# Kernel tuning notes

Measured on AMD Instinct MI355X. Metric: run time of the kernel, lower is better.

The kernel has to match this reference:

```python
import jax, jax.numpy as jnp
import numpy as np

TEMPERATURE = 0.5  # init temperature; attn_drop=0.0 so dropout is identity


def setup_inputs() -> dict:
    key = jax.random.key(0)
    k1, k2, k3 = jax.random.split(key, 3)
    B, H, N, D = 4, 8, 2048, 64
    q = jax.random.normal(k1, (B, H, N, D), dtype=jnp.float32)
    k = jax.random.normal(k2, (B, H, N, D), dtype=jnp.float32)
    v = jax.random.normal(k3, (B, H, N, D), dtype=jnp.float32)
    scale = jnp.asarray(D ** -0.5, dtype=jnp.float32)
    return {"q": q, "k": k, "v": v, "scale": scale}


def reference(q, k, v, scale):
    # logits: [B,H,N,N]
    logits = jnp.einsum("bhqd,bhkd->bhqk", q, k) * scale
    # first softmax acts as a soft mask over keys
    soft_mask = jax.nn.softmax(logits / TEMPERATURE, axis=-1)
    # second softmax over masked logits (elementwise product, NOT matmul)
    attn = jax.nn.softmax(logits * soft_mask, axis=-1)
    # dropout with p=0.0 is identity
    out = jnp.einsum("bhqk,bhkd->bhqd", attn, v)
    return out
```

## Files before the change

kernel.cpp:

```cpp
#include <hip/hip_runtime.h>


typedef _Float16 f16;
typedef f16 f16x8 __attribute__((ext_vector_type(8)));
typedef float f32x4 __attribute__((ext_vector_type(4)));

#define MFMA(a, b, c) __builtin_amdgcn_mfma_f32_16x16x32_f16((a), (b), (c), 0, 0, 0)
#define EXP2(x) __builtin_amdgcn_exp2f(x)

#define N_CTX 2048
#define DH 64
#define KT 64
#define NKT (N_CTX / KT)
#define ROWS 128
#define QS 72

#define C2  2.885390081777927f
#define L2E 1.442695040888963f

__device__ inline unsigned pk(float a, float b) {
    typedef __fp16 fp16x2_t __attribute__((ext_vector_type(2)));
    union { fp16x2_t v; unsigned u; } x;
    x.v = __builtin_amdgcn_cvt_pkrtz(a, b);
    return x.u;
}

__global__ __launch_bounds__(512, 4)
void stk_attn_mfma(const float* __restrict__ qg, const float* __restrict__ kg,
                   const float* __restrict__ vglob, const float* __restrict__ sg,
                   float* __restrict__ og) {
    __shared__ f16 Qs[ROWS * QS];
    __shared__ f16 Ks[KT * QS];
    __shared__ f16 Vt[DH * KT];
    __shared__ f16 Ps[8][16 * KT];

    const int tid  = threadIdx.x;
    const int wv   = tid >> 6;
    const int lane = tid & 63;
    const int l15  = lane & 15;
    const int q4   = lane >> 4;
    const int vp   = tid & 31;
    const int vgr  = tid >> 5;
    const int bh   = blockIdx.x & 31;
    const int q0   = (blockIdx.x >> 5) * ROWS;
    const float scale = sg[0];

    const float* qb = qg + (size_t)bh * N_CTX * DH;
    const float* kb = kg + (size_t)bh * N_CTX * DH;
    const float* vb = vglob + (size_t)bh * N_CTX * DH;
    float*       ob = og + (size_t)bh * N_CTX * DH;

    #pragma unroll
    for (int it = 0; it < 4; ++it) {
        int idx = it * 512 + tid;
        int row = idx >> 4, c4 = idx & 15;
        float4 v = *(const float4*)&qb[((size_t)(q0 + row)) * DH + c4 * 4];
        *(uint2*)&Qs[row * QS + c4 * 4] =
            make_uint2(pk(v.x * scale, v.y * scale), pk(v.z * scale, v.w * scale));
    }
    __syncthreads();

    f16x8 aq[2];
    #pragma unroll
    for (int kc = 0; kc < 2; ++kc)
        aq[kc] = *(const f16x8*)&Qs[(wv * 16 + l15) * QS + kc * 32 + q4 * 8];

    float s1[4] = {0, 0, 0, 0};
    float4 kr[2];
    #pragma unroll
    for (int it = 0; it < 2; ++it) {
        int idx = it * 512 + tid;
        kr[it] = *(const float4*)&kb[((size_t)(idx >> 4)) * DH + (idx & 15) * 4];
    }
    for (int kt = 0; kt < NKT; ++kt) {
        __syncthreads();
        #pragma unroll
        for (int it = 0; it < 2; ++it) {
            int idx = it * 512 + tid;
            int row = idx >> 4, c4 = idx & 15;
            *(uint2*)&Ks[row * QS + c4 * 4] =
                make_uint2(pk(kr[it].x, kr[it].y), pk(kr[it].z, kr[it].w));
        }
        __syncthreads();
        if (kt + 1 < NKT) {
            #pragma unroll
            for (int it = 0; it < 2; ++it) {
                int idx = it * 512 + tid;
                kr[it] = *(const float4*)&kb[((size_t)(kt + 1) * KT + (idx >> 4)) * DH + (idx & 15) * 4];
            }
        }
        #pragma unroll
        for (int kgi = 0; kgi < 4; ++kgi) {
            f16x8 b0 = *(const f16x8*)&Ks[(kgi * 16 + l15) * QS + 0 * 32 + q4 * 8];
            f16x8 b1 = *(const f16x8*)&Ks[(kgi * 16 + l15) * QS + 1 * 32 + q4 * 8];
            f32x4 acc = {0.f, 0.f, 0.f, 0.f};
            acc = MFMA(aq[0], b0, acc);
            acc = MFMA(aq[1], b1, acc);
            #pragma unroll
            for (int r = 0; r < 4; ++r)
                s1[r] += EXP2(acc[r] * C2);
        }
    }
    float inv1[4];
    #pragma unroll
    for (int s = 0; s < 4; ++s) {
        float v = s1[s];
        v += __shfl_xor(v, 1, 64);
        v += __shfl_xor(v, 2, 64);
        v += __shfl_xor(v, 4, 64);
        v += __shfl_xor(v, 8, 64);
        inv1[s] = L2E / v;
    }

    float l2[4] = {0, 0, 0, 0};
    f32x4 O[4];
    #pragma unroll
    for (int dt = 0; dt < 4; ++dt) O[dt] = (f32x4){0.f, 0.f, 0.f, 0.f};

    float4 vr[2];
    #pragma unroll
    for (int it = 0; it < 2; ++it) {
        int idx = it * 512 + tid;
        kr[it] = *(const float4*)&kb[((size_t)(idx >> 4)) * DH + (idx & 15) * 4];
    }
    {
        const float* vs = vb + ((size_t)2 * vp) * DH + vgr * 4;
        vr[0] = *(const float4*)(vs);
        vr[1] = *(const float4*)(vs + DH);
    }
    for (int kt = 0; kt < NKT; ++kt) {
        __syncthreads();
        #pragma unroll
        for (int it = 0; it < 2; ++it) {
            int idx = it * 512 + tid;
            int row = idx >> 4, c4 = idx & 15;
            *(uint2*)&Ks[row * QS + c4 * 4] =
                make_uint2(pk(kr[it].x, kr[it].y), pk(kr[it].z, kr[it].w));
        }
        #pragma unroll
        for (int j = 0; j < 4; ++j) {
            int d = vgr * 4 + j;
            float a0 = ((const float*)&vr[0])[j];
            float a1 = ((const float*)&vr[1])[j];
            *(unsigned*)&Vt[d * KT + ((2 * vp) ^ (8 * (d & 7)))] = pk(a0, a1);
        }
        __syncthreads();
        if (kt + 1 < NKT) {
            #pragma unroll
            for (int it = 0; it < 2; ++it) {
                int idx = it * 512 + tid;
                kr[it] = *(const float4*)&kb[((size_t)(kt + 1) * KT + (idx >> 4)) * DH + (idx & 15) * 4];
            }
            const float* vs = vb + ((size_t)(kt + 1) * KT + 2 * vp) * DH + vgr * 4;
            vr[0] = *(const float4*)(vs);
            vr[1] = *(const float4*)(vs + DH);
        }

        #pragma unroll
        for (int kgi = 0; kgi < 4; ++kgi) {
            f16x8 b0 = *(const f16x8*)&Ks[(kgi * 16 + l15) * QS + 0 * 32 + q4 * 8];
            f16x8 b1 = *(const f16x8*)&Ks[(kgi * 16 + l15) * QS + 1 * 32 + q4 * 8];
            f32x4 acc = {0.f, 0.f, 0.f, 0.f};
            acc = MFMA(aq[0], b0, acc);
            acc = MFMA(aq[1], b1, acc);
            #pragma unroll
            for (int r = 0; r < 4; ++r) {
                float L  = acc[r];
                float e1 = EXP2(L * C2);
                float e2 = EXP2((L * e1) * inv1[r]);
                l2[r] += e2;
                int lrow = q4 * 4 + r;
                int col  = kgi * 16 + l15;
                Ps[wv][lrow * KT + (col ^ ((lrow & 7) * 8))] = (f16)e2;
            }
        }
        #pragma unroll
        for (int kc = 0; kc < 2; ++kc) {
            int kbase = kc * 32 + q4 * 8;
            f16x8 ap = *(const f16x8*)&Ps[wv][l15 * KT + (kbase ^ ((l15 & 7) * 8))];
            #pragma unroll
            for (int dt = 0; dt < 4; ++dt) {
                f16x8 bv = *(const f16x8*)&Vt[(dt * 16 + l15) * KT + (kbase ^ ((l15 & 7) * 8))];
                O[dt] = MFMA(ap, bv, O[dt]);
            }
        }
    }

    float invl2[4];
    #pragma unroll
    for (int s = 0; s < 4; ++s) {
        float v = l2[s];
        v += __shfl_xor(v, 1, 64);
        v += __shfl_xor(v, 2, 64);
        v += __shfl_xor(v, 4, 64);
        v += __shfl_xor(v, 8, 64);
        invl2[s] = 1.0f / v;
    }
    #pragma unroll
    for (int dt = 0; dt < 4; ++dt)
        #pragma unroll
        for (int r = 0; r < 4; ++r) {
            int row = q0 + wv * 16 + q4 * 4 + r;
            ob[(size_t)row * DH + dt * 16 + l15] = O[dt][r] * invl2[r];
        }
}

extern "C" void kernel_launch(void* const* d_in, const int* in_sizes, int n_in,
                              void* d_out, int out_size, void* d_ws, size_t ws_size,
                              hipStream_t stream) {
    const float* q = (const float*)d_in[0];
    const float* k = (const float*)d_in[1];
    const float* v = (const float*)d_in[2];
    const float* s = (const float*)d_in[3];
    float* out = (float*)d_out;
    dim3 grid(32 * 16);
    stk_attn_mfma<<<grid, 512, 0, stream>>>(q, k, v, s, out);
}
```

Measured before the change: 181.7 us.

## Double-buffer K tiles in shared memory and cut per-tile barriers

Both passes now keep two K tiles in shared memory, so the next tile can be written while the current one is read by MFMAs. This lets the first pass drop to one barrier per tile. Global prefetch of K now runs two tiles ahead, and the V prefetch is moved after the QK compute. The second pass still has two barriers per tile because Vt is single-buffered. The cost is more LDS (an extra K tile), more live registers, and clamped redundant loads on the final tiles.

```diff
diff --git a/kernel.cpp b/kernel.cpp
--- a/kernel.cpp
+++ b/kernel.cpp
@@ -30,7 +30,7 @@
                    const float* __restrict__ vglob, const float* __restrict__ sg,
                    float* __restrict__ og) {
     __shared__ f16 Qs[ROWS * QS];
-    __shared__ f16 Ks[KT * QS];
+    __shared__ f16 Ks[2][KT * QS];
     __shared__ f16 Vt[DH * KT];
     __shared__ f16 Ps[8][16 * KT];
 
@@ -72,27 +72,39 @@
         int idx = it * 512 + tid;
         kr[it] = *(const float4*)&kb[((size_t)(idx >> 4)) * DH + (idx & 15) * 4];
     }
+    #pragma unroll
+    for (int it = 0; it < 2; ++it) {
+        int idx = it * 512 + tid;
+        *(uint2*)&Ks[0][(idx >> 4) * QS + (idx & 15) * 4] =
+            make_uint2(pk(kr[it].x, kr[it].y), pk(kr[it].z, kr[it].w));
+    }
+    #pragma unroll
+    for (int it = 0; it < 2; ++it) {
+        int idx = it * 512 + tid;
+        kr[it] = *(const float4*)&kb[((size_t)KT + (idx >> 4)) * DH + (idx & 15) * 4];
+    }
+    __syncthreads();
+
     for (int kt = 0; kt < NKT; ++kt) {
-        __syncthreads();
+        const int cur = kt & 1, nxt = cur ^ 1;
         #pragma unroll
         for (int it = 0; it < 2; ++it) {
             int idx = it * 512 + tid;
-            int row = idx >> 4, c4 = idx & 15;
-            *(uint2*)&Ks[row * QS + c4 * 4] =
+            *(uint2*)&Ks[nxt][(idx >> 4) * QS + (idx & 15) * 4] =
                 make_uint2(pk(kr[it].x, kr[it].y), pk(kr[it].z, kr[it].w));
         }
-        __syncthreads();
-        if (kt + 1 < NKT) {
+        {
+            int tn = (kt + 2 < NKT) ? kt + 2 : NKT - 1;
             #pragma unroll
             for (int it = 0; it < 2; ++it) {
                 int idx = it * 512 + tid;
-                kr[it] = *(const float4*)&kb[((size_t)(kt + 1) * KT + (idx >> 4)) * DH + (idx & 15) * 4];
+                kr[it] = *(const float4*)&kb[((size_t)tn * KT + (idx >> 4)) * DH + (idx & 15) * 4];
             }
         }
         #pragma unroll
         for (int kgi = 0; kgi < 4; ++kgi) {
-            f16x8 b0 = *(const f16x8*)&Ks[(kgi * 16 + l15) * QS + 0 * 32 + q4 * 8];
-            f16x8 b1 = *(const f16x8*)&Ks[(kgi * 16 + l15) * QS + 1 * 32 + q4 * 8];
+            f16x8 b0 = *(const f16x8*)&Ks[cur][(kgi * 16 + l15) * QS + 0 * 32 + q4 * 8];
+            f16x8 b1 = *(const f16x8*)&Ks[cur][(kgi * 16 + l15) * QS + 1 * 32 + q4 * 8];
             f32x4 acc = {0.f, 0.f, 0.f, 0.f};
             acc = MFMA(aq[0], b0, acc);
             acc = MFMA(aq[1], b1, acc);
@@ -100,6 +112,7 @@
             for (int r = 0; r < 4; ++r)
                 s1[r] += EXP2(acc[r] * C2);
         }
+        __syncthreads();
     }
     float inv1[4];
     #pragma unroll
@@ -123,20 +136,26 @@
         int idx = it * 512 + tid;
         kr[it] = *(const float4*)&kb[((size_t)(idx >> 4)) * DH + (idx & 15) * 4];
     }
+    #pragma unroll
+    for (int it = 0; it < 2; ++it) {
+        int idx = it * 512 + tid;
+        *(uint2*)&Ks[0][(idx >> 4) * QS + (idx & 15) * 4] =
+            make_uint2(pk(kr[it].x, kr[it].y), pk(kr[it].z, kr[it].w));
+    }
     {
         const float* vs = vb + ((size_t)2 * vp) * DH + vgr * 4;
         vr[0] = *(const float4*)(vs);
         vr[1] = *(const float4*)(vs + DH);
     }
+    #pragma unroll
+    for (int it = 0; it < 2; ++it) {
+        int idx = it * 512 + tid;
+        kr[it] = *(const float4*)&kb[((size_t)KT + (idx >> 4)) * DH + (idx & 15) * 4];
+    }
+    __syncthreads();
+
     for (int kt = 0; kt < NKT; ++kt) {
-        __syncthreads();
-        #pragma unroll
-        for (int it = 0; it < 2; ++it) {
-            int idx = it * 512 + tid;
-            int row = idx >> 4, c4 = idx & 15;
-            *(uint2*)&Ks[row * QS + c4 * 4] =
-                make_uint2(pk(kr[it].x, kr[it].y), pk(kr[it].z, kr[it].w));
-        }
+        const int cur = kt & 1, nxt = cur ^ 1;
         #pragma unroll
         for (int j = 0; j < 4; ++j) {
             int d = vgr * 4 + j;
@@ -144,22 +163,16 @@
             float a1 = ((const float*)&vr[1])[j];
             *(unsigned*)&Vt[d * KT + ((2 * vp) ^ (8 * (d & 7)))] = pk(a0, a1);
         }
-        __syncthreads();
-        if (kt + 1 < NKT) {
-            #pragma unroll
-            for (int it = 0; it < 2; ++it) {
-                int idx = it * 512 + tid;
-                kr[it] = *(const float4*)&kb[((size_t)(kt + 1) * KT + (idx >> 4)) * DH + (idx & 15) * 4];
-            }
-            const float* vs = vb + ((size_t)(kt + 1) * KT + 2 * vp) * DH + vgr * 4;
-            vr[0] = *(const float4*)(vs);
-            vr[1] = *(const float4*)(vs + DH);
-        }
-
+        #pragma unroll
+        for (int it = 0; it < 2; ++it) {
+            int idx = it * 512 + tid;
+            *(uint2*)&Ks[nxt][(idx >> 4) * QS + (idx & 15) * 4] =
+                make_uint2(pk(kr[it].x, kr[it].y), pk(kr[it].z, kr[it].w));
+        }
         #pragma unroll
         for (int kgi = 0; kgi < 4; ++kgi) {
-            f16x8 b0 = *(const f16x8*)&Ks[(kgi * 16 + l15) * QS + 0 * 32 + q4 * 8];
-            f16x8 b1 = *(const f16x8*)&Ks[(kgi * 16 + l15) * QS + 1 * 32 + q4 * 8];
+            f16x8 b0 = *(const f16x8*)&Ks[cur][(kgi * 16 + l15) * QS + 0 * 32 + q4 * 8];
+            f16x8 b1 = *(const f16x8*)&Ks[cur][(kgi * 16 + l15) * QS + 1 * 32 + q4 * 8];
             f32x4 acc = {0.f, 0.f, 0.f, 0.f};
             acc = MFMA(aq[0], b0, acc);
             acc = MFMA(aq[1], b1, acc);
@@ -174,6 +187,19 @@
                 Ps[wv][lrow * KT + (col ^ ((lrow & 7) * 8))] = (f16)e2;
             }
         }
+        {
+            int tv = (kt + 1 < NKT) ? kt + 1 : NKT - 1;
+            int tk = (kt + 2 < NKT) ? kt + 2 : NKT - 1;
+            const float* vs = vb + ((size_t)tv * KT + 2 * vp) * DH + vgr * 4;
+            vr[0] = *(const float4*)(vs);
+            vr[1] = *(const float4*)(vs + DH);
+            #pragma unroll
+            for (int it = 0; it < 2; ++it) {
+                int idx = it * 512 + tid;
+                kr[it] = *(const float4*)&kb[((size_t)tk * KT + (idx >> 4)) * DH + (idx & 15) * 4];
+            }
+        }
+        __syncthreads();
         #pragma unroll
         for (int kc = 0; kc < 2; ++kc) {
             int kbase = kc * 32 + q4 * 8;
@@ -184,6 +210,7 @@
                 O[dt] = MFMA(ap, bv, O[dt]);
             }
         }
+        __syncthreads();
     }
 
     float invl2[4];
```

New measurement: 173.9 us. 4.3% less time.

## Pre-convert K and transposed V to fp16, stream tiles via direct global-to-LDS loads

Applied to the files above, without the earlier changes.

Adds two prepass kernels: one converts K to fp16 and one writes V to fp16 in transposed layout, both into the workspace. The attention kernel then loads K and V^T tiles with global_load_lds into double-buffered, XOR-swizzled LDS, replacing the register staging and per-tile fp32-to-fp16 conversion. The temperature factor is folded into the Q scale so one multiply per logit goes away. Each K/V tile is now read at half the bytes by the 16 query blocks per head, at the cost of two extra launches and an extra round trip through memory for K and V.

```diff
diff --git a/kernel.cpp b/kernel.cpp
--- a/kernel.cpp
+++ b/kernel.cpp
@@ -14,9 +14,9 @@
 #define NKT (N_CTX / KT)
 #define ROWS 128
 #define QS 72
-
-#define C2  2.885390081777927f
-#define L2E 1.442695040888963f
+#define HEAD_ELEMS (N_CTX * DH)
+
+#define C2 2.885390081777927f
 
 __device__ inline unsigned pk(float a, float b) {
     typedef __fp16 fp16x2_t __attribute__((ext_vector_type(2)));
@@ -25,30 +25,68 @@
     return x.u;
 }
 
+__device__ inline void load16_lds(const f16* g, f16* l) {
+    __builtin_amdgcn_global_load_lds(
+        (const __attribute__((address_space(1))) void*)g,
+        (__attribute__((address_space(3))) void*)l, 16, 0, 0);
+}
+
+__global__ __launch_bounds__(256)
+void cvt_k(const float* __restrict__ k, f16* __restrict__ out) {
+    int i = (blockIdx.x * 256 + threadIdx.x) * 8;
+    float4 a = *(const float4*)&k[i];
+    float4 b = *(const float4*)&k[i + 4];
+    uint4 r = make_uint4(pk(a.x, a.y), pk(a.z, a.w), pk(b.x, b.y), pk(b.z, b.w));
+    *(uint4*)&out[i] = r;
+}
+
+__global__ __launch_bounds__(256)
+void cvt_vt(const float* __restrict__ v, f16* __restrict__ out) {
+    __shared__ float Vs[64][65];
+    const int bh = blockIdx.x >> 5;
+    const int kt = blockIdx.x & 31;
+    const int t  = threadIdx.x;
+    const float* vb = v + (size_t)bh * HEAD_ELEMS + (size_t)kt * KT * DH;
+    #pragma unroll
+    for (int it = 0; it < 4; ++it) {
+        int idx = it * 256 + t;
+        int row = idx >> 4, c4 = idx & 15;
+        float4 x = *(const float4*)&vb[row * DH + c4 * 4];
+        *(float4*)&Vs[row][c4 * 4] = x;
+    }
+    __syncthreads();
+    int d = t >> 2, kq = t & 3;
+    unsigned w[8];
+    #pragma unroll
+    for (int j = 0; j < 8; ++j)
+        w[j] = pk(Vs[kq * 16 + 2 * j][d], Vs[kq * 16 + 2 * j + 1][d]);
+    f16* ob = out + (size_t)bh * HEAD_ELEMS + (size_t)d * N_CTX + kt * KT + kq * 16;
+    *(uint4*)(ob)     = make_uint4(w[0], w[1], w[2], w[3]);
+    *(uint4*)(ob + 8) = make_uint4(w[4], w[5], w[6], w[7]);
+}
+
 __global__ __launch_bounds__(512, 4)
-void stk_attn_mfma(const float* __restrict__ qg, const float* __restrict__ kg,
-                   const float* __restrict__ vglob, const float* __restrict__ sg,
+void stk_attn_mfma(const float* __restrict__ qg, const f16* __restrict__ kh,
+                   const f16* __restrict__ vth, const float* __restrict__ sg,
                    float* __restrict__ og) {
     __shared__ f16 Qs[ROWS * QS];
-    __shared__ f16 Ks[KT * QS];
-    __shared__ f16 Vt[DH * KT];
-    __shared__ f16 Ps[8][16 * KT];
+    __shared__ f16 Ks[2][KT * DH];
+    __shared__ f16 Vt[2][DH * KT];
+    __shared__ f16 Ps[8][16 * QS];
 
     const int tid  = threadIdx.x;
     const int wv   = tid >> 6;
     const int lane = tid & 63;
     const int l15  = lane & 15;
     const int q4   = lane >> 4;
-    const int vp   = tid & 31;
-    const int vgr  = tid >> 5;
     const int bh   = blockIdx.x & 31;
     const int q0   = (blockIdx.x >> 5) * ROWS;
-    const float scale = sg[0];
-
-    const float* qb = qg + (size_t)bh * N_CTX * DH;
-    const float* kb = kg + (size_t)bh * N_CTX * DH;
-    const float* vb = vglob + (size_t)bh * N_CTX * DH;
-    float*       ob = og + (size_t)bh * N_CTX * DH;
+    const float scale2 = sg[0] * C2;
+
+    const float* qb = qg + (size_t)bh * HEAD_ELEMS;
+    const f16*   kb = kh + (size_t)bh * HEAD_ELEMS;
+    const f16*   vtb = vth + (size_t)bh * HEAD_ELEMS;
+    float*       ob = og + (size_t)bh * HEAD_ELEMS;
 
     #pragma unroll
     for (int it = 0; it < 4; ++it) {
@@ -56,7 +94,7 @@
         int row = idx >> 4, c4 = idx & 15;
         float4 v = *(const float4*)&qb[((size_t)(q0 + row)) * DH + c4 * 4];
         *(uint2*)&Qs[row * QS + c4 * 4] =
-            make_uint2(pk(v.x * scale, v.y * scale), pk(v.z * scale, v.w * scale));
+            make_uint2(pk(v.x * scale2, v.y * scale2), pk(v.z * scale2, v.w * scale2));
     }
     __syncthreads();
 
@@ -65,41 +103,39 @@
     for (int kc = 0; kc < 2; ++kc)
         aq[kc] = *(const f16x8*)&Qs[(wv * 16 + l15) * QS + kc * 32 + q4 * 8];
 
+    const int kc_   = wv * 64 + lane;
+    const int kkey  = kc_ >> 3;
+    const int kdl   = (kc_ & 7) ^ (kkey & 7);
+    const int ks_src = kkey * DH + kdl * 8;
+    const long vt_src = (long)kkey * N_CTX + kdl * 8;
+    f16* const ks_dst0 = &Ks[0][wv * 512];
+    f16* const vt_dst0 = &Vt[0][wv * 512];
+    const int ko0 = l15 * 64 + ((q4 ^ (l15 & 7)) * 8);
+    const int ko1 = l15 * 64 + (((q4 + 4) ^ (l15 & 7)) * 8);
+    const int vo0 = l15 * 64 + ((q4 ^ (l15 & 7)) * 8);
+    const int vo1 = l15 * 64 + (((4 + q4) ^ (l15 & 7)) * 8);
+    f16* const ps_w = &Ps[wv][(q4 * 4) * QS + l15];
+    const f16* const ps_r = &Ps[wv][l15 * QS + q4 * 8];
+
     float s1[4] = {0, 0, 0, 0};
-    float4 kr[2];
-    #pragma unroll
-    for (int it = 0; it < 2; ++it) {
-        int idx = it * 512 + tid;
-        kr[it] = *(const float4*)&kb[((size_t)(idx >> 4)) * DH + (idx & 15) * 4];
-    }
+    load16_lds(kb + ks_src, ks_dst0);
+    __syncthreads();
     for (int kt = 0; kt < NKT; ++kt) {
-        __syncthreads();
-        #pragma unroll
-        for (int it = 0; it < 2; ++it) {
-            int idx = it * 512 + tid;
-            int row = idx >> 4, c4 = idx & 15;
-            *(uint2*)&Ks[row * QS + c4 * 4] =
-                make_uint2(pk(kr[it].x, kr[it].y), pk(kr[it].z, kr[it].w));
-        }
-        __syncthreads();
-        if (kt + 1 < NKT) {
-            #pragma unroll
-            for (int it = 0; it < 2; ++it) {
-                int idx = it * 512 + tid;
-                kr[it] = *(const float4*)&kb[((size_t)(kt + 1) * KT + (idx >> 4)) * DH + (idx & 15) * 4];
-            }
-        }
+        const int cur = kt & 1;
+        if (kt + 1 < NKT)
+            load16_lds(kb + (kt + 1) * (KT * DH) + ks_src, ks_dst0 + (cur ^ 1) * (KT * DH));
         #pragma unroll
         for (int kgi = 0; kgi < 4; ++kgi) {
-            f16x8 b0 = *(const f16x8*)&Ks[(kgi * 16 + l15) * QS + 0 * 32 + q4 * 8];
-            f16x8 b1 = *(const f16x8*)&Ks[(kgi * 16 + l15) * QS + 1 * 32 + q4 * 8];
+            f16x8 b0 = *(const f16x8*)&Ks[cur][kgi * 1024 + ko0];
+            f16x8 b1 = *(const f16x8*)&Ks[cur][kgi * 1024 + ko1];
             f32x4 acc = {0.f, 0.f, 0.f, 0.f};
             acc = MFMA(aq[0], b0, acc);
             acc = MFMA(aq[1], b1, acc);
             #pragma unroll
             for (int r = 0; r < 4; ++r)
-                s1[r] += EXP2(acc[r] * C2);
-        }
+                s1[r] += EXP2(acc[r]);
+        }
+        __syncthreads();
     }
     float inv1[4];
     #pragma unroll
@@ -109,7 +145,7 @@
         v += __shfl_xor(v, 2, 64);
         v += __shfl_xor(v, 4, 64);
         v += __shfl_xor(v, 8, 64);
-        inv1[s] = L2E / v;
+        inv1[s] = 0.5f / v;
     }
 
     float l2[4] = {0, 0, 0, 0};
@@ -117,73 +153,42 @@
     #pragma unroll
     for (int dt = 0; dt < 4; ++dt) O[dt] = (f32x4){0.f, 0.f, 0.f, 0.f};
 
-    float4 vr[2];
-    #pragma unroll
-    for (int it = 0; it < 2; ++it) {
-        int idx = it * 512 + tid;
-        kr[it] = *(const float4*)&kb[((size_t)(idx >> 4)) * DH + (idx & 15) * 4];
-    }
-    {
-        const float* vs = vb + ((size_t)2 * vp) * DH + vgr * 4;
-        vr[0] = *(const float4*)(vs);
-        vr[1] = *(const float4*)(vs + DH);
-    }
+    load16_lds(kb + ks_src, ks_dst0);
+    load16_lds(vtb + vt_src, vt_dst0);
+    __syncthreads();
     for (int kt = 0; kt < NKT; ++kt) {
-        __syncthreads();
-        #pragma unroll
-        for (int it = 0; it < 2; ++it) {
-            int idx = it * 512 + tid;
-            int row = idx >> 4, c4 = idx & 15;
-            *(uint2*)&Ks[row * QS + c4 * 4] =
-                make_uint2(pk(kr[it].x, kr[it].y), pk(kr[it].z, kr[it].w));
-        }
-        #pragma unroll
-        for (int j = 0; j < 4; ++j) {
-            int d = vgr * 4 + j;
-            float a0 = ((const float*)&vr[0])[j];
-            float a1 = ((const float*)&vr[1])[j];
-            *(unsigned*)&Vt[d * KT + ((2 * vp) ^ (8 * (d & 7)))] = pk(a0, a1);
-        }
-        __syncthreads();
+        const int cur = kt & 1;
         if (kt + 1 < NKT) {
-            #pragma unroll
-            for (int it = 0; it < 2; ++it) {
-                int idx = it * 512 + tid;
-                kr[it] = *(const float4*)&kb[((size_t)(kt + 1) * KT + (idx >> 4)) * DH + (idx & 15) * 4];
-            }
-            const float* vs = vb + ((size_t)(kt + 1) * KT + 2 * vp) * DH + vgr * 4;
-            vr[0] = *(const float4*)(vs);
-            vr[1] = *(const float4*)(vs + DH);
-        }
-
+            load16_lds(kb + (kt + 1) * (KT * DH) + ks_src, ks_dst0 + (cur ^ 1) * (KT * DH));
+            load16_lds(vtb + vt_src + (kt + 1) * KT, vt_dst0 + (cur ^ 1) * (DH * KT));
+        }
         #pragma unroll
         for (int kgi = 0; kgi < 4; ++kgi) {
-            f16x8 b0 = *(const f16x8*)&Ks[(kgi * 16 + l15) * QS + 0 * 32 + q4 * 8];
-            f16x8 b1 = *(const f16x8*)&Ks[(kgi * 16 + l15) * QS + 1 * 32 + q4 * 8];
+            f16x8 b0 = *(const f16x8*)&Ks[cur][kgi * 1024 + ko0];
+            f16x8 b1 = *(const f16x8*)&Ks[cur][kgi * 1024 + ko1];
             f32x4 acc = {0.f, 0.f, 0.f, 0.f};
             acc = MFMA(aq[0], b0, acc);
             acc = MFMA(aq[1], b1, acc);
             #pragma unroll
             for (int r = 0; r < 4; ++r) {
-                float L  = acc[r];
-                float e1 = EXP2(L * C2);
-                float e2 = EXP2((L * e1) * inv1[r]);
+                float a  = acc[r];
+                float e1 = EXP2(a);
+                float e2 = EXP2((a * e1) * inv1[r]);
                 l2[r] += e2;
-                int lrow = q4 * 4 + r;
-                int col  = kgi * 16 + l15;
-                Ps[wv][lrow * KT + (col ^ ((lrow & 7) * 8))] = (f16)e2;
+                ps_w[r * QS + kgi * 16] = (f16)e2;
             }
         }
         #pragma unroll
         for (int kc = 0; kc < 2; ++kc) {
-            int kbase = kc * 32 + q4 * 8;
-            f16x8 ap = *(const f16x8*)&Ps[wv][l15 * KT + (kbase ^ ((l15 & 7) * 8))];
+            f16x8 ap = *(const f16x8*)&ps_r[kc * 32];
+            const int vo = (kc == 0) ? vo0 : vo1;
             #pragma unroll
             for (int dt = 0; dt < 4; ++dt) {
-                f16x8 bv = *(const f16x8*)&Vt[(dt * 16 + l15) * KT + (kbase ^ ((l15 & 7) * 8))];
+                f16x8 bv = *(const f16x8*)&Vt[cur][dt * 1024 + vo];
                 O[dt] = MFMA(ap, bv, O[dt]);
             }
         }
+        __syncthreads();
     }
 
     float invl2[4];
@@ -213,6 +218,10 @@
     const float* v = (const float*)d_in[2];
     const float* s = (const float*)d_in[3];
     float* out = (float*)d_out;
+    f16* kf = (f16*)d_ws;
+    f16* vtf = (f16*)((char*)d_ws + 8388608);
+    cvt_k<<<2048, 256, 0, stream>>>(k, kf);
+    cvt_vt<<<1024, 256, 0, stream>>>(v, vtf);
     dim3 grid(32 * 16);
-    stk_attn_mfma<<<grid, 512, 0, stream>>>(q, k, v, s, out);
-}
+    stk_attn_mfma<<<grid, 512, 0, stream>>>(q, kf, vtf, s, out);
+}
```

Result: faster. 175.9 us (-3.2%).
